# Optimization experiments

Hardware: AMD Instinct MI355X
Metric: run time of the kernel (lower is better)

## Reference

```python
import jax, jax.numpy as jnp
import numpy as np
from jax import lax

DIM = 1024
N = 8192

def setup_inputs() -> dict:
    key = jax.random.key(0)
    ks = jax.random.split(key, 7)
    ifeats = jax.random.normal(ks[0], (N, DIM), dtype=jnp.float32)
    tfeat_n = jax.random.normal(ks[1], (1, DIM), dtype=jnp.float32)
    tfeat_a = jax.random.normal(ks[2], (1, DIM), dtype=jnp.float32)
    # Conv2d(1, 2, kernel_size=(3,5), padding=(0,2)) params, OIHW
    fan_in_c = 1 * 3 * 5
    bc = 1.0 / np.sqrt(fan_in_c)
    conv_w = jax.random.uniform(ks[3], (2, 1, 3, 5), minval=-bc, maxval=bc, dtype=jnp.float32)
    conv_b = jax.random.uniform(ks[4], (2,), minval=-bc, maxval=bc, dtype=jnp.float32)
    # Linear(2*dim, dim)
    bl = 1.0 / np.sqrt(2 * DIM)
    w2 = jax.random.uniform(ks[5], (DIM, 2 * DIM), minval=-bl, maxval=bl, dtype=jnp.float32)
    b2 = jax.random.uniform(ks[6], (DIM,), minval=-bl, maxval=bl, dtype=jnp.float32)
    return {"ifeats": ifeats, "tfeat_n": tfeat_n, "tfeat_a": tfeat_a,
            "conv_w": conv_w, "conv_b": conv_b, "w2": w2, "b2": b2}

def reference(ifeats, tfeat_n, tfeat_a, conv_w, conv_b, w2, b2):
    n, d = ifeats.shape
    # Batch the per-sample loop: feats_i = [tfeat_n; tfeat_a; ifeats[i]] -> [N,1,3,D]
    tn = jnp.broadcast_to(tfeat_n, (n, d))
    ta = jnp.broadcast_to(tfeat_a, (n, d))
    x1 = jnp.stack([tn, ta, ifeats], axis=1)[:, None]  # [N,1,3,D]
    # Conv2d(1->2, k=(3,5), pad=(0,2)): height collapses 3->1, width D preserved
    x2 = lax.conv_general_dilated(x1, conv_w, window_strides=(1, 1),
                                  padding=((0, 0), (2, 2)),
                                  dimension_numbers=("NCHW", "OIHW", "NCHW"))
    x2 = x2 + conv_b[None, :, None, None]              # [N,2,1,D]
    x2 = jax.nn.gelu(x2, approximate=False)            # torch nn.GELU() is exact
    x2 = x2.reshape(n, 2 * d)                          # channel-major flatten, matches view(1,-1)
    x3 = x2 @ w2.T + b2                                # Linear(2D -> D)
    return ifeats + x3
```

## Files before the change

kernel.cpp:

```cpp
#include <hip/hip_runtime.h>
#include <cstdint>

#define DIMD 1024
#define NROWS 8192
#define KDIM 2048

typedef unsigned short u16;
typedef __bf16 bf16x8 __attribute__((ext_vector_type(8)));
typedef float f32x4 __attribute__((ext_vector_type(4)));

__device__ __forceinline__ u16 f2bf(float f) {
  unsigned u = __builtin_bit_cast(unsigned, f);
  return (u16)((u + 0x7FFFu + ((u >> 16) & 1u)) >> 16);
}

__device__ __forceinline__ float gelu_exact(float x) {
  float s = 0.70710678118654752f * x;
  float a = fabsf(s);
  float k = __fdividef(1.0f, fmaf(0.3275911f, a, 1.0f));
  float p = 1.061405429f;
  p = fmaf(p, k, -1.453152027f);
  p = fmaf(p, k, 1.421413741f);
  p = fmaf(p, k, -0.284496736f);
  p = fmaf(p, k, 0.254829592f);
  p = p * k;
  float e = __expf(-s * s);
  float erf_s = copysignf(fmaf(-p, e, 1.0f), s);
  return 0.5f * x * (1.0f + erf_s);
}

__global__ __launch_bounds__(256) void pre_kernel(
    const float* __restrict__ ifeats, const float* __restrict__ tn,
    const float* __restrict__ ta, const float* __restrict__ cw,
    const float* __restrict__ cb, const float* __restrict__ w2,
    u16* __restrict__ x2, u16* __restrict__ w2b) {
  const int b = blockIdx.x;
  const int t = threadIdx.x;
  if (b < NROWS) {
    __shared__ float si[DIMD], sn[DIMD], sa[DIMD];
    ((float4*)si)[t] = ((const float4*)(ifeats + (size_t)b * DIMD))[t];
    ((float4*)sn)[t] = ((const float4*)tn)[t];
    ((float4*)sa)[t] = ((const float4*)ta)[t];
    __syncthreads();
    const int c = t >> 7;
    const int w0 = (t & 127) << 3;
    float cwn[5], cwa[5], cwi[5];
#pragma unroll
    for (int k = 0; k < 5; ++k) {
      cwn[k] = cw[c * 15 + k];
      cwa[k] = cw[c * 15 + 5 + k];
      cwi[k] = cw[c * 15 + 10 + k];
    }
    const float bias = cb[c];
    float wn[12], wa[12], wi[12];
#pragma unroll
    for (int j = 0; j < 12; ++j) {
      int wp = w0 - 2 + j;
      bool ok = (wp >= 0) && (wp < DIMD);
      wn[j] = ok ? sn[wp] : 0.f;
      wa[j] = ok ? sa[wp] : 0.f;
      wi[j] = ok ? si[wp] : 0.f;
    }
    union { u16 o[8]; uint4 u; } pk;
#pragma unroll
    for (int s = 0; s < 8; ++s) {
      float x = bias;
#pragma unroll
      for (int k = 0; k < 5; ++k) {
        x = fmaf(cwn[k], wn[s + k], x);
        x = fmaf(cwa[k], wa[s + k], x);
        x = fmaf(cwi[k], wi[s + k], x);
      }
      pk.o[s] = f2bf(gelu_exact(x));
    }
    *(uint4*)(x2 + (size_t)b * KDIM + c * DIMD + w0) = pk.u;
  } else {
    const int t2 = (b - NROWS) * 256 + t;
    const float4* p = (const float4*)(w2 + (size_t)t2 * 8);
    float4 a = p[0], bb = p[1];
    union { u16 o[8]; uint4 v; } pk;
    pk.o[0] = f2bf(a.x);  pk.o[1] = f2bf(a.y);  pk.o[2] = f2bf(a.z);  pk.o[3] = f2bf(a.w);
    pk.o[4] = f2bf(bb.x); pk.o[5] = f2bf(bb.y); pk.o[6] = f2bf(bb.z); pk.o[7] = f2bf(bb.w);
    *(uint4*)(w2b + (size_t)t2 * 8) = pk.v;
  }
}

__device__ __forceinline__ void gl_lds16(const u16* g, u16* l) {
  __builtin_amdgcn_global_load_lds(
      (__attribute__((address_space(1))) void*)g,
      (__attribute__((address_space(3))) void*)l, 16, 0, 0);
}

#define BK 64

__global__ __launch_bounds__(512, 4) void gemm_bt(
    const u16* __restrict__ A,
    const u16* __restrict__ B,
    const float* __restrict__ ifeats,
    const float* __restrict__ b2,
    float* __restrict__ out) {
  constexpr int K = KDIM;
  __shared__ __align__(16) u16 sA[2][128 * BK];
  __shared__ __align__(16) u16 sB[2][128 * BK];

  const int tid = threadIdx.x;
  const int wv = tid >> 6;
  const int lane = tid & 63;
  const int id = blockIdx.x;
  const int xcd = id & 7;
  const int s_ = id >> 3;
  const int i0 = (xcd * 8 + (s_ >> 3)) * 128;
  const int j0 = (s_ & 7) * 128;

  const int wm = (wv & 1) * 64;
  const int wn = (wv >> 1) * 32;
  const int quad = lane >> 4;
  const int r16 = lane & 15;
  const int sw = r16 & 7;

  const int srow = lane >> 3;
  const int schunk = (lane & 7) ^ srow;
  const u16* gA[2];
  const u16* gB[2];
#pragma unroll
  for (int i = 0; i < 2; ++i) {
    int r = wv * 16 + i * 8 + srow;
    gA[i] = A + (size_t)(i0 + r) * K + schunk * 8;
    gB[i] = B + (size_t)(j0 + r) * K + schunk * 8;
  }

  const f32x4 vzero = {0.f, 0.f, 0.f, 0.f};
  f32x4 acc[4][2];
#pragma unroll
  for (int a = 0; a < 4; ++a)
#pragma unroll
    for (int b = 0; b < 2; ++b) acc[a][b] = vzero;

  auto stage = [&](int buf, int k0) {
#pragma unroll
    for (int i = 0; i < 2; ++i) {
      u16* la = &sA[buf][(wv * 16 + i * 8) * BK];
      u16* lb = &sB[buf][(wv * 16 + i * 8) * BK];
      gl_lds16(gA[i] + k0, la);
      gl_lds16(gB[i] + k0, lb);
    }
  };

  auto compute = [&](int buf) {
#pragma unroll
    for (int s = 0; s < 2; ++s) {
      bf16x8 av[4], bv[2];
#pragma unroll
      for (int mt = 0; mt < 4; ++mt)
        av[mt] = *(const bf16x8*)&sA[buf][(wm + mt * 16 + r16) * BK + (((s * 4 + quad) ^ sw) << 3)];
#pragma unroll
      for (int nt = 0; nt < 2; ++nt)
        bv[nt] = *(const bf16x8*)&sB[buf][(wn + nt * 16 + r16) * BK + (((s * 4 + quad) ^ sw) << 3)];
#pragma unroll
      for (int mt = 0; mt < 4; ++mt)
#pragma unroll
        for (int nt = 0; nt < 2; ++nt)
          acc[mt][nt] = __builtin_amdgcn_mfma_f32_16x16x32_bf16(av[mt], bv[nt], acc[mt][nt], 0, 0, 0);
    }
  };

  stage(0, 0);
  for (int k0 = 0; k0 < K; k0 += 2 * BK) {
    __syncthreads();
    if (k0 + BK < K) stage(1, k0 + BK);
    compute(0);
    __syncthreads();
    if (k0 + 2 * BK < K) stage(0, k0 + 2 * BK);
    compute(1);
  }

#pragma unroll
  for (int nt = 0; nt < 2; ++nt) {
    int col = j0 + wn + nt * 16 + r16;
    float bias = b2[col];
#pragma unroll
    for (int mt = 0; mt < 4; ++mt) {
      int rbase = i0 + wm + mt * 16 + quad * 4;
#pragma unroll
      for (int r = 0; r < 4; ++r) {
        size_t idx = (size_t)(rbase + r) * DIMD + col;
        out[idx] = ifeats[idx] + bias + acc[mt][nt][r];
      }
    }
  }
}

extern "C" void kernel_launch(void* const* d_in, const int* in_sizes, int n_in,
                              void* d_out, int out_size, void* d_ws, size_t ws_size,
                              hipStream_t stream) {
  const float* ifeats = (const float*)d_in[0];
  const float* tn     = (const float*)d_in[1];
  const float* ta     = (const float*)d_in[2];
  const float* cw     = (const float*)d_in[3];
  const float* cb     = (const float*)d_in[4];
  const float* w2     = (const float*)d_in[5];
  const float* b2     = (const float*)d_in[6];
  float* out = (float*)d_out;

  u16* w2b = (u16*)d_ws;
  u16* x2  = (u16*)((char*)d_ws + (size_t)DIMD * KDIM * 2);

  pre_kernel<<<NROWS + (DIMD * KDIM / 8) / 256, 256, 0, stream>>>(
      ifeats, tn, ta, cw, cb, w2, x2, w2b);
  gemm_bt<<<512, 512, 0, stream>>>(x2, w2b, ifeats, b2, out);
}
```

Before: 159.9 us.

## Restructure GEMM into triple-buffered 4-wave pipeline with split prefetch and priority hints

Rewrites the bf16 GEMM main loop so it uses 256 threads (4 waves), each computing a 64x64 sub-tile, with a K step of 32 and three LDS buffers. Global-to-LDS loads run two tiles ahead and are split into A and B halves interleaved between MFMA groups. The loop uses explicit vmcnt waits, s_barrier, and setprio to overlap memory with compute and cut per-iteration sync overhead. The trade-offs are more accumulator registers per wave, fewer waves per block, and a hand-tuned barrier and waitcnt schedule that is fragile.

```diff
diff --git a/kernel.cpp b/kernel.cpp
--- a/kernel.cpp
+++ b/kernel.cpp
@@ -91,17 +91,17 @@
       (__attribute__((address_space(3))) void*)l, 16, 0, 0);
 }
 
-#define BK 64
-
-__global__ __launch_bounds__(512, 4) void gemm_bt(
+#define BK 32
+#define NTILE 64
+
+__global__ __launch_bounds__(256, 2) void gemm_bt(
     const u16* __restrict__ A,
     const u16* __restrict__ B,
     const float* __restrict__ ifeats,
     const float* __restrict__ b2,
     float* __restrict__ out) {
-  constexpr int K = KDIM;
-  __shared__ __align__(16) u16 sA[2][128 * BK];
-  __shared__ __align__(16) u16 sB[2][128 * BK];
+  __shared__ __align__(16) u16 sA[3][128 * BK];
+  __shared__ __align__(16) u16 sB[3][128 * BK];
 
   const int tid = threadIdx.x;
   const int wv = tid >> 6;
@@ -113,69 +113,91 @@
   const int j0 = (s_ & 7) * 128;
 
   const int wm = (wv & 1) * 64;
-  const int wn = (wv >> 1) * 32;
+  const int wn = (wv >> 1) * 64;
   const int quad = lane >> 4;
   const int r16 = lane & 15;
-  const int sw = r16 & 7;
-
-  const int srow = lane >> 3;
-  const int schunk = (lane & 7) ^ srow;
+  const int csw = (r16 >> 1) & 3;
+
+  const int grow = tid >> 2;
+  const int gchk = (tid & 3) ^ ((tid >> 3) & 3);
   const u16* gA[2];
   const u16* gB[2];
 #pragma unroll
-  for (int i = 0; i < 2; ++i) {
-    int r = wv * 16 + i * 8 + srow;
-    gA[i] = A + (size_t)(i0 + r) * K + schunk * 8;
-    gB[i] = B + (size_t)(j0 + r) * K + schunk * 8;
-  }
+  for (int u = 0; u < 2; ++u) {
+    gA[u] = A + (size_t)(i0 + u * 64 + grow) * KDIM + gchk * 8;
+    gB[u] = B + (size_t)(j0 + u * 64 + grow) * KDIM + gchk * 8;
+  }
+  const int ldsoff = wv * 16 * BK;
 
   const f32x4 vzero = {0.f, 0.f, 0.f, 0.f};
-  f32x4 acc[4][2];
+  f32x4 acc[4][4];
 #pragma unroll
   for (int a = 0; a < 4; ++a)
 #pragma unroll
-    for (int b = 0; b < 2; ++b) acc[a][b] = vzero;
-
-  auto stage = [&](int buf, int k0) {
-#pragma unroll
-    for (int i = 0; i < 2; ++i) {
-      u16* la = &sA[buf][(wv * 16 + i * 8) * BK];
-      u16* lb = &sB[buf][(wv * 16 + i * 8) * BK];
-      gl_lds16(gA[i] + k0, la);
-      gl_lds16(gB[i] + k0, lb);
-    }
+    for (int b = 0; b < 4; ++b) acc[a][b] = vzero;
+
+  u16* a0 = (u16*)sA[0]; u16* a1 = (u16*)sA[1]; u16* a2 = (u16*)sA[2];
+  u16* b0 = (u16*)sB[0]; u16* b1 = (u16*)sB[1]; u16* b2s = (u16*)sB[2];
+
+  auto issueA = [&](u16* buf, int t, int u) {
+    gl_lds16(gA[u] + t * BK, buf + u * 64 * BK + ldsoff);
   };
-
-  auto compute = [&](int buf) {
-#pragma unroll
-    for (int s = 0; s < 2; ++s) {
-      bf16x8 av[4], bv[2];
-#pragma unroll
-      for (int mt = 0; mt < 4; ++mt)
-        av[mt] = *(const bf16x8*)&sA[buf][(wm + mt * 16 + r16) * BK + (((s * 4 + quad) ^ sw) << 3)];
-#pragma unroll
-      for (int nt = 0; nt < 2; ++nt)
-        bv[nt] = *(const bf16x8*)&sB[buf][(wn + nt * 16 + r16) * BK + (((s * 4 + quad) ^ sw) << 3)];
-#pragma unroll
-      for (int mt = 0; mt < 4; ++mt)
-#pragma unroll
-        for (int nt = 0; nt < 2; ++nt)
-          acc[mt][nt] = __builtin_amdgcn_mfma_f32_16x16x32_bf16(av[mt], bv[nt], acc[mt][nt], 0, 0, 0);
-    }
+  auto issueB = [&](u16* buf, int t, int u) {
+    gl_lds16(gB[u] + t * BK, buf + u * 64 * BK + ldsoff);
   };
-
-  stage(0, 0);
-  for (int k0 = 0; k0 < K; k0 += 2 * BK) {
-    __syncthreads();
-    if (k0 + BK < K) stage(1, k0 + BK);
-    compute(0);
-    __syncthreads();
-    if (k0 + 2 * BK < K) stage(0, k0 + 2 * BK);
-    compute(1);
-  }
-
-#pragma unroll
-  for (int nt = 0; nt < 2; ++nt) {
+  auto ldfrag = [&](const u16* buf, int row) -> bf16x8 {
+    return *(const bf16x8*)&buf[(row + r16) * BK + ((quad ^ csw) << 3)];
+  };
+
+  issueA(a0, 0, 0); issueA(a0, 0, 1); issueB(b0, 0, 0); issueB(b0, 0, 1);
+  issueA(a1, 1, 0); issueA(a1, 1, 1); issueB(b1, 1, 0); issueB(b1, 1, 1);
+  asm volatile("s_waitcnt vmcnt(4)" ::: "memory");
+  __builtin_amdgcn_s_barrier();
+
+  for (int t = 0; t < NTILE; ++t) {
+    const bool pf = (t + 2) < NTILE;
+    bf16x8 av0 = ldfrag(a0, wm);
+    bf16x8 av1 = ldfrag(a0, wm + 16);
+    bf16x8 bv0 = ldfrag(b0, wn);
+    bf16x8 bv1 = ldfrag(b0, wn + 16);
+    bf16x8 bv2 = ldfrag(b0, wn + 32);
+    bf16x8 bv3 = ldfrag(b0, wn + 48);
+    if (pf) { issueA(a2, t + 2, 0); issueA(a2, t + 2, 1); }
+    __builtin_amdgcn_s_barrier();
+    __builtin_amdgcn_s_setprio(1);
+    acc[0][0] = __builtin_amdgcn_mfma_f32_16x16x32_bf16(av0, bv0, acc[0][0], 0, 0, 0);
+    acc[0][1] = __builtin_amdgcn_mfma_f32_16x16x32_bf16(av0, bv1, acc[0][1], 0, 0, 0);
+    acc[0][2] = __builtin_amdgcn_mfma_f32_16x16x32_bf16(av0, bv2, acc[0][2], 0, 0, 0);
+    acc[0][3] = __builtin_amdgcn_mfma_f32_16x16x32_bf16(av0, bv3, acc[0][3], 0, 0, 0);
+    acc[1][0] = __builtin_amdgcn_mfma_f32_16x16x32_bf16(av1, bv0, acc[1][0], 0, 0, 0);
+    acc[1][1] = __builtin_amdgcn_mfma_f32_16x16x32_bf16(av1, bv1, acc[1][1], 0, 0, 0);
+    acc[1][2] = __builtin_amdgcn_mfma_f32_16x16x32_bf16(av1, bv2, acc[1][2], 0, 0, 0);
+    acc[1][3] = __builtin_amdgcn_mfma_f32_16x16x32_bf16(av1, bv3, acc[1][3], 0, 0, 0);
+    __builtin_amdgcn_s_setprio(0);
+    __builtin_amdgcn_s_barrier();
+    bf16x8 av2 = ldfrag(a0, wm + 32);
+    bf16x8 av3 = ldfrag(a0, wm + 48);
+    if (pf) { issueB(b2s, t + 2, 0); issueB(b2s, t + 2, 1); }
+    __builtin_amdgcn_s_barrier();
+    __builtin_amdgcn_s_setprio(1);
+    acc[2][0] = __builtin_amdgcn_mfma_f32_16x16x32_bf16(av2, bv0, acc[2][0], 0, 0, 0);
+    acc[2][1] = __builtin_amdgcn_mfma_f32_16x16x32_bf16(av2, bv1, acc[2][1], 0, 0, 0);
+    acc[2][2] = __builtin_amdgcn_mfma_f32_16x16x32_bf16(av2, bv2, acc[2][2], 0, 0, 0);
+    acc[2][3] = __builtin_amdgcn_mfma_f32_16x16x32_bf16(av2, bv3, acc[2][3], 0, 0, 0);
+    acc[3][0] = __builtin_amdgcn_mfma_f32_16x16x32_bf16(av3, bv0, acc[3][0], 0, 0, 0);
+    acc[3][1] = __builtin_amdgcn_mfma_f32_16x16x32_bf16(av3, bv1, acc[3][1], 0, 0, 0);
+    acc[3][2] = __builtin_amdgcn_mfma_f32_16x16x32_bf16(av3, bv2, acc[3][2], 0, 0, 0);
+    acc[3][3] = __builtin_amdgcn_mfma_f32_16x16x32_bf16(av3, bv3, acc[3][3], 0, 0, 0);
+    __builtin_amdgcn_s_setprio(0);
+    if (pf) asm volatile("s_waitcnt vmcnt(4)" ::: "memory");
+    else    asm volatile("s_waitcnt vmcnt(0)" ::: "memory");
+    __builtin_amdgcn_s_barrier();
+    u16* ta_ = a0; a0 = a1; a1 = a2; a2 = ta_;
+    u16* tb_ = b0; b0 = b1; b1 = b2s; b2s = tb_;
+  }
+
+#pragma unroll
+  for (int nt = 0; nt < 4; ++nt) {
     int col = j0 + wn + nt * 16 + r16;
     float bias = b2[col];
 #pragma unroll
@@ -207,5 +229,5 @@
 
   pre_kernel<<<NROWS + (DIMD * KDIM / 8) / 256, 256, 0, stream>>>(
       ifeats, tn, ta, cw, cb, w2, x2, w2b);
-  gemm_bt<<<512, 512, 0, stream>>>(x2, w2b, ifeats, b2, out);
-}
+  gemm_bt<<<512, 256, 0, stream>>>(x2, w2b, ifeats, b2, out);
+}
```

Result: slower. 165.8 us (+3.7%).

## Use triple-buffered BK=32 pipeline with 4 waves and larger per-wave tiles

Applied to the files above, without the earlier changes.

The GEMM now runs 4 waves of 256 threads per block instead of 8, and each wave computes a 64x64 sub-tile. K steps drop to 32 and the LDS staging becomes a 3-deep ring of buffers, with explicit vmcnt waits so loads for tile t+2 overlap the MFMA work on tile t. The LDS swizzle is recomputed for the narrower rows. The aim is better latency hiding and more register reuse per LDS read, at the cost of higher register pressure and lower occupancy. There are also twice as many barriers per unit of K work.

```diff
diff --git a/kernel.cpp b/kernel.cpp
--- a/kernel.cpp
+++ b/kernel.cpp
@@ -91,17 +91,18 @@
       (__attribute__((address_space(3))) void*)l, 16, 0, 0);
 }
 
-#define BK 64
-
-__global__ __launch_bounds__(512, 4) void gemm_bt(
+#define BK 32
+#define NTILE 64
+
+__global__ __launch_bounds__(256, 3) void gemm_bt(
     const u16* __restrict__ A,
     const u16* __restrict__ B,
     const float* __restrict__ ifeats,
     const float* __restrict__ b2,
     float* __restrict__ out) {
   constexpr int K = KDIM;
-  __shared__ __align__(16) u16 sA[2][128 * BK];
-  __shared__ __align__(16) u16 sB[2][128 * BK];
+  __shared__ __align__(16) u16 sA[3][128 * BK];
+  __shared__ __align__(16) u16 sB[3][128 * BK];
 
   const int tid = threadIdx.x;
   const int wv = tid >> 6;
@@ -113,69 +114,76 @@
   const int j0 = (s_ & 7) * 128;
 
   const int wm = (wv & 1) * 64;
-  const int wn = (wv >> 1) * 32;
+  const int wn = (wv >> 1) * 64;
   const int quad = lane >> 4;
   const int r16 = lane & 15;
-  const int sw = r16 & 7;
-
-  const int srow = lane >> 3;
-  const int schunk = (lane & 7) ^ srow;
+  const int csw = (r16 >> 1) & 3;
+
+  const int srow = lane >> 2;
+  const int schk = (lane & 3) ^ ((lane >> 3) & 3);
   const u16* gA[2];
   const u16* gB[2];
 #pragma unroll
-  for (int i = 0; i < 2; ++i) {
-    int r = wv * 16 + i * 8 + srow;
-    gA[i] = A + (size_t)(i0 + r) * K + schunk * 8;
-    gB[i] = B + (size_t)(j0 + r) * K + schunk * 8;
-  }
+  for (int u = 0; u < 2; ++u) {
+    gA[u] = A + (size_t)(i0 + u * 64 + wv * 16 + srow) * K + schk * 8;
+    gB[u] = B + (size_t)(j0 + u * 64 + wv * 16 + srow) * K + schk * 8;
+  }
+  const int ldso = wv * 16 * BK;
 
   const f32x4 vzero = {0.f, 0.f, 0.f, 0.f};
-  f32x4 acc[4][2];
+  f32x4 acc[4][4];
 #pragma unroll
   for (int a = 0; a < 4; ++a)
 #pragma unroll
-    for (int b = 0; b < 2; ++b) acc[a][b] = vzero;
-
-  auto stage = [&](int buf, int k0) {
-#pragma unroll
-    for (int i = 0; i < 2; ++i) {
-      u16* la = &sA[buf][(wv * 16 + i * 8) * BK];
-      u16* lb = &sB[buf][(wv * 16 + i * 8) * BK];
-      gl_lds16(gA[i] + k0, la);
-      gl_lds16(gB[i] + k0, lb);
+    for (int b = 0; b < 4; ++b) acc[a][b] = vzero;
+
+  u16* a0 = (u16*)sA[0]; u16* a1 = (u16*)sA[1]; u16* a2 = (u16*)sA[2];
+  u16* b0 = (u16*)sB[0]; u16* b1 = (u16*)sB[1]; u16* b2s = (u16*)sB[2];
+
+  auto issue = [&](u16* bufA, u16* bufB, int t) {
+#pragma unroll
+    for (int u = 0; u < 2; ++u) {
+      gl_lds16(gA[u] + t * BK, bufA + u * 64 * BK + ldso);
+      gl_lds16(gB[u] + t * BK, bufB + u * 64 * BK + ldso);
     }
   };
 
-  auto compute = [&](int buf) {
-#pragma unroll
-    for (int s = 0; s < 2; ++s) {
-      bf16x8 av[4], bv[2];
-#pragma unroll
-      for (int mt = 0; mt < 4; ++mt)
-        av[mt] = *(const bf16x8*)&sA[buf][(wm + mt * 16 + r16) * BK + (((s * 4 + quad) ^ sw) << 3)];
-#pragma unroll
-      for (int nt = 0; nt < 2; ++nt)
-        bv[nt] = *(const bf16x8*)&sB[buf][(wn + nt * 16 + r16) * BK + (((s * 4 + quad) ^ sw) << 3)];
-#pragma unroll
-      for (int mt = 0; mt < 4; ++mt)
-#pragma unroll
-        for (int nt = 0; nt < 2; ++nt)
-          acc[mt][nt] = __builtin_amdgcn_mfma_f32_16x16x32_bf16(av[mt], bv[nt], acc[mt][nt], 0, 0, 0);
-    }
-  };
-
-  stage(0, 0);
-  for (int k0 = 0; k0 < K; k0 += 2 * BK) {
-    __syncthreads();
-    if (k0 + BK < K) stage(1, k0 + BK);
-    compute(0);
-    __syncthreads();
-    if (k0 + 2 * BK < K) stage(0, k0 + 2 * BK);
-    compute(1);
-  }
-
-#pragma unroll
-  for (int nt = 0; nt < 2; ++nt) {
+  issue(a0, b0, 0);
+  issue(a1, b1, 1);
+
+  for (int t = 0; t < NTILE; ++t) {
+    __builtin_amdgcn_s_barrier();
+    __builtin_amdgcn_sched_barrier(0);
+    if (t + 2 < NTILE) issue(a2, b2s, t + 2);
+    if (t + 2 < NTILE) {
+      asm volatile("s_waitcnt vmcnt(8)" ::: "memory");
+    } else if (t + 1 < NTILE) {
+      asm volatile("s_waitcnt vmcnt(4)" ::: "memory");
+    } else {
+      asm volatile("s_waitcnt vmcnt(0)" ::: "memory");
+    }
+    __builtin_amdgcn_s_barrier();
+    __builtin_amdgcn_sched_barrier(0);
+
+    bf16x8 av[4], bv[4];
+#pragma unroll
+    for (int mt = 0; mt < 4; ++mt)
+      av[mt] = *(const bf16x8*)&a0[(wm + mt * 16 + r16) * BK + ((quad ^ csw) << 3)];
+#pragma unroll
+    for (int nt = 0; nt < 4; ++nt)
+      bv[nt] = *(const bf16x8*)&b0[(wn + nt * 16 + r16) * BK + ((quad ^ csw) << 3)];
+#pragma unroll
+    for (int mt = 0; mt < 4; ++mt)
+#pragma unroll
+      for (int nt = 0; nt < 4; ++nt)
+        acc[mt][nt] = __builtin_amdgcn_mfma_f32_16x16x32_bf16(av[mt], bv[nt], acc[mt][nt], 0, 0, 0);
+
+    u16* ta_ = a0; a0 = a1; a1 = a2; a2 = ta_;
+    u16* tb_ = b0; b0 = b1; b1 = b2s; b2s = tb_;
+  }
+
+#pragma unroll
+  for (int nt = 0; nt < 4; ++nt) {
     int col = j0 + wn + nt * 16 + r16;
     float bias = b2[col];
 #pragma unroll
@@ -207,5 +215,5 @@
 
   pre_kernel<<<NROWS + (DIMD * KDIM / 8) / 256, 256, 0, stream>>>(
       ifeats, tn, ta, cw, cb, w2, x2, w2b);
-  gemm_bt<<<512, 512, 0, stream>>>(x2, w2b, ifeats, b2, out);
-}
+  gemm_bt<<<512, 256, 0, stream>>>(x2, w2b, ifeats, b2, out);
+}
```

Result: slower. 168.1 us (+5.1%).

## Hoist row-invariant conv taps and process 8 rows per block in pre-kernel

Applied to the files above, without the earlier changes.

The conv contribution from the broadcast tfeat_n/tfeat_a rows is identical for every sample, so it is now computed once per thread and reused across 8 rows per block. The shared-memory staging and barrier are removed, and ifeats is read straight from global memory with vector loads plus edge scalars. This also cuts the grid from 8192+1024 blocks to 2048. The cost is less parallelism per block and a serial row loop, which could expose global load latency.

```diff
diff --git a/kernel.cpp b/kernel.cpp
--- a/kernel.cpp
+++ b/kernel.cpp
@@ -36,12 +36,7 @@
     u16* __restrict__ x2, u16* __restrict__ w2b) {
   const int b = blockIdx.x;
   const int t = threadIdx.x;
-  if (b < NROWS) {
-    __shared__ float si[DIMD], sn[DIMD], sa[DIMD];
-    ((float4*)si)[t] = ((const float4*)(ifeats + (size_t)b * DIMD))[t];
-    ((float4*)sn)[t] = ((const float4*)tn)[t];
-    ((float4*)sa)[t] = ((const float4*)ta)[t];
-    __syncthreads();
+  if (b < 1024) {
     const int c = t >> 7;
     const int w0 = (t & 127) << 3;
     float cwn[5], cwa[5], cwi[5];
@@ -52,30 +47,54 @@
       cwi[k] = cw[c * 15 + 10 + k];
     }
     const float bias = cb[c];
-    float wn[12], wa[12], wi[12];
-#pragma unroll
-    for (int j = 0; j < 12; ++j) {
-      int wp = w0 - 2 + j;
-      bool ok = (wp >= 0) && (wp < DIMD);
-      wn[j] = ok ? sn[wp] : 0.f;
-      wa[j] = ok ? sa[wp] : 0.f;
-      wi[j] = ok ? si[wp] : 0.f;
-    }
-    union { u16 o[8]; uint4 u; } pk;
-#pragma unroll
-    for (int s = 0; s < 8; ++s) {
-      float x = bias;
-#pragma unroll
-      for (int k = 0; k < 5; ++k) {
-        x = fmaf(cwn[k], wn[s + k], x);
-        x = fmaf(cwa[k], wa[s + k], x);
-        x = fmaf(cwi[k], wi[s + k], x);
-      }
-      pk.o[s] = f2bf(gelu_exact(x));
-    }
-    *(uint4*)(x2 + (size_t)b * KDIM + c * DIMD + w0) = pk.u;
+    float base[8];
+    {
+      float wn[12], wa[12];
+#pragma unroll
+      for (int j = 0; j < 12; ++j) {
+        int wp = w0 - 2 + j;
+        bool ok = (wp >= 0) && (wp < DIMD);
+        wn[j] = ok ? tn[ok ? wp : 0] : 0.f;
+        wa[j] = ok ? ta[ok ? wp : 0] : 0.f;
+      }
+#pragma unroll
+      for (int s = 0; s < 8; ++s) {
+        float x = bias;
+#pragma unroll
+        for (int k = 0; k < 5; ++k) {
+          x = fmaf(cwn[k], wn[s + k], x);
+          x = fmaf(cwa[k], wa[s + k], x);
+        }
+        base[s] = x;
+      }
+    }
+    const bool has_l = (w0 > 0);
+    const bool has_r = (w0 < DIMD - 8);
+#pragma unroll 1
+    for (int r = 0; r < 8; ++r) {
+      const int row = b * 8 + r;
+      const float* irow = ifeats + (size_t)row * DIMD;
+      float wi[12];
+      float4 m0 = *(const float4*)(irow + w0);
+      float4 m1 = *(const float4*)(irow + w0 + 4);
+      wi[0] = has_l ? irow[w0 - 2] : 0.f;
+      wi[1] = has_l ? irow[w0 - 1] : 0.f;
+      wi[2] = m0.x; wi[3] = m0.y; wi[4] = m0.z; wi[5] = m0.w;
+      wi[6] = m1.x; wi[7] = m1.y; wi[8] = m1.z; wi[9] = m1.w;
+      wi[10] = has_r ? irow[w0 + 8] : 0.f;
+      wi[11] = has_r ? irow[w0 + 9] : 0.f;
+      union { u16 o[8]; uint4 u; } pk;
+#pragma unroll
+      for (int s = 0; s < 8; ++s) {
+        float x = base[s];
+#pragma unroll
+        for (int k = 0; k < 5; ++k) x = fmaf(cwi[k], wi[s + k], x);
+        pk.o[s] = f2bf(gelu_exact(x));
+      }
+      *(uint4*)(x2 + (size_t)row * KDIM + c * DIMD + w0) = pk.u;
+    }
   } else {
-    const int t2 = (b - NROWS) * 256 + t;
+    const int t2 = (b - 1024) * 256 + t;
     const float4* p = (const float4*)(w2 + (size_t)t2 * 8);
     float4 a = p[0], bb = p[1];
     union { u16 o[8]; uint4 v; } pk;
@@ -205,7 +224,6 @@
   u16* w2b = (u16*)d_ws;
   u16* x2  = (u16*)((char*)d_ws + (size_t)DIMD * KDIM * 2);
 
-  pre_kernel<<<NROWS + (DIMD * KDIM / 8) / 256, 256, 0, stream>>>(
-      ifeats, tn, ta, cw, cb, w2, x2, w2b);
+  pre_kernel<<<2048, 256, 0, stream>>>(ifeats, tn, ta, cw, cb, w2, x2, w2b);
   gemm_bt<<<512, 512, 0, stream>>>(x2, w2b, ifeats, b2, out);
 }
```

Measured after the change: 158.0 us. About the same (-1.2%).
